# Kernel optimization log

Measured on AMD Instinct MI355X. Metric: run time of the kernel, lower is better.

## Reference

```python
import jax, jax.numpy as jnp
import numpy as np

B, T, C, H = 2, 2048, 1024, 16
D = C // H  # head dim


def setup_inputs() -> dict:
    key = jax.random.key(0)
    ks = jax.random.split(key, 8)
    s = 1.0 / np.sqrt(C)
    return {
        "x_q": jax.random.normal(ks[0], (B, T, C), jnp.float32),
        "x_kv": jax.random.normal(ks[1], (B, T, C), jnp.float32),
        "Wq": jax.random.normal(ks[2], (C, C), jnp.float32) * s,
        "bq": jnp.zeros((C,), jnp.float32),
        "Wkv": jax.random.normal(ks[3], (C, 2 * C), jnp.float32) * s,
        "bkv": jnp.zeros((2 * C,), jnp.float32),
        "Wo": jax.random.normal(ks[4], (C, C), jnp.float32) * s,
        "bo": jnp.zeros((C,), jnp.float32),
    }


def reference(x_q, x_kv, Wq, bq, Wkv, bkv, Wo, bo):
    q = x_q @ Wq + bq                      # [B,Tq,C]
    kv = x_kv @ Wkv + bkv                  # [B,Tkv,2C]
    k, v = kv[..., :C], kv[..., C:]
    # split heads -> [B,H,T,D]
    q = q.reshape(B, T, H, D).transpose(0, 2, 1, 3)
    k = k.reshape(B, T, H, D).transpose(0, 2, 1, 3)
    v = v.reshape(B, T, H, D).transpose(0, 2, 1, 3)
    att = jnp.einsum("bhqd,bhkd->bhqk", q, k) * (1.0 / np.sqrt(D))
    att = jax.nn.softmax(att, axis=-1)
    y = jnp.einsum("bhqk,bhkd->bhqd", att, v)
    y = y.transpose(0, 2, 1, 3).reshape(B, T, C)
    return y @ Wo + bo
```

## Files before the change

### kernel.cpp

```cpp
#include <hip/hip_runtime.h>

#define NB 2
#define NT 2048
#define NC 1024
#define NH 16
#define ND 64
#define NC2 2048
#define QSCALE (0.125f * 1.4426950408889634f)

typedef __attribute__((ext_vector_type(8))) __bf16 bf16x8;
typedef __attribute__((ext_vector_type(8))) unsigned short ushort8;
typedef __attribute__((ext_vector_type(4))) float f32x4;

__device__ __forceinline__ unsigned short bf16_bits(float f) {
  union { float f; unsigned int u; } x; x.f = f;
  unsigned int r = x.u + 0x7fffu + ((x.u >> 16) & 1u);
  return (unsigned short)(r >> 16);
}
__device__ __forceinline__ float bf2f(unsigned short u) {
  union { unsigned int u; float f; } x; x.u = ((unsigned int)u) << 16;
  return x.f;
}
__device__ __forceinline__ void g2l16(const void* g, void* l) {
  __builtin_amdgcn_global_load_lds(
      (const __attribute__((address_space(1))) unsigned int*)g,
      (__attribute__((address_space(3))) unsigned int*)l, 16, 0, 0);
}
__device__ __forceinline__ bf16x8 ld8(const unsigned short* p) {
  return *(const bf16x8*)p;
}
__device__ __forceinline__ unsigned int cvtpk(float lo, float hi) {
  unsigned int r;
  asm("v_cvt_pk_bf16_f32 %0, %1, %2" : "=v"(r) : "v"(lo), "v"(hi));
  return r;
}
__device__ __forceinline__ float vexp2(float x) {
  float r;
  asm("v_exp_f32 %0, %1" : "=v"(r) : "v"(x));
  return r;
}

__device__ __forceinline__ int wave_is_f32(const unsigned short* __restrict__ x) {
  const int lane = threadIdx.x & 63;
  ulonglong2 v = ((const ulonglong2*)x)[lane];
  const unsigned short* u = (const unsigned short*)&v;
  int c = 0;
#pragma unroll
  for (int k = 0; k < 8; ++k) {
    int e = (u[k] >> 7) & 0xFF;
    c += (e != 0 && (e < 112 || e > 142)) ? 1 : 0;
  }
#pragma unroll
  for (int off = 32; off > 0; off >>= 1) c += __shfl_down(c, off);
  return __shfl(c, 0) > 64;
}

__global__ __launch_bounds__(256) void prep(const void* __restrict__ xq,
                                            const void* __restrict__ xkv,
                                            const void* __restrict__ w0,
                                            const void* __restrict__ w1,
                                            const void* __restrict__ w2,
                                            unsigned short* __restrict__ oq,
                                            unsigned short* __restrict__ okv,
                                            unsigned short* __restrict__ o0,
                                            unsigned short* __restrict__ o1,
                                            unsigned short* __restrict__ o2) {
  __shared__ unsigned short tile[32][33];
  const int bx = blockIdx.x, by = blockIdx.y;
  const int f = wave_is_f32((const unsigned short*)xq);
  if (bx < 128) {
    if (!f) return;
    const int fb = bx * 32 + by;
    const void* in = (fb < 2048) ? xq : xkv;
    unsigned short* out = (fb < 2048) ? oq : okv;
    const int i = (fb & 2047) * 256 + threadIdx.x;
    const float4* p = (const float4*)in;
    float4 a = p[i * 2], b = p[i * 2 + 1];
    ushort8 o;
    o[0] = bf16_bits(a.x); o[1] = bf16_bits(a.y); o[2] = bf16_bits(a.z); o[3] = bf16_bits(a.w);
    o[4] = bf16_bits(b.x); o[5] = bf16_bits(b.y); o[6] = bf16_bits(b.z); o[7] = bf16_bits(b.w);
    *(ushort8*)&out[(size_t)i * 8] = o;
  } else {
    const int tb = bx - 128;
    const void* in; unsigned short* out; int cols, cb;
    if (tb < 32)      { in = w0; out = o0; cols = NC;  cb = tb; }
    else if (tb < 96) { in = w1; out = o1; cols = NC2; cb = tb - 32; }
    else              { in = w2; out = o2; cols = NC;  cb = tb - 96; }
    const int c0 = cb * 32, r0 = by * 32;
    const int tx = threadIdx.x & 31, ty = threadIdx.x >> 5;
#pragma unroll
    for (int i = 0; i < 32; i += 8) {
      size_t idx = (size_t)(r0 + ty + i) * cols + c0 + tx;
      tile[ty + i][tx] = f ? bf16_bits(((const float*)in)[idx]) : ((const unsigned short*)in)[idx];
    }
    __syncthreads();
#pragma unroll
    for (int i = 0; i < 32; i += 8)
      out[(size_t)(c0 + ty + i) * NC + r0 + tx] = tile[tx][ty + i];
  }
}

__global__ __launch_bounds__(256) void gemm_qkv(const unsigned short* __restrict__ xq_raw,
                                                const unsigned short* __restrict__ xkv_raw,
                                                const unsigned short* __restrict__ xq_cvt,
                                                const unsigned short* __restrict__ xkv_cvt,
                                                const unsigned short* __restrict__ Wqt,
                                                const unsigned short* __restrict__ Wkvt,
                                                const void* __restrict__ bq,
                                                const void* __restrict__ bkv,
                                                unsigned short* __restrict__ qb,
                                                unsigned short* __restrict__ kf2,
                                                unsigned short* __restrict__ vt2) {
  __shared__ unsigned short As[128][64];
  __shared__ unsigned short Bs[128][64];
  const int f = wave_is_f32(xq_raw);
  const bool isq = blockIdx.y < 8;
  const unsigned short* A  = isq ? (f ? xq_cvt : xq_raw) : (f ? xkv_cvt : xkv_raw);
  const unsigned short* Bt = isq ? Wqt : Wkvt;
  const int m0 = blockIdx.x * 128;
  const int n0 = (isq ? blockIdx.y : blockIdx.y - 8) * 128;
  const int tid = threadIdx.x, w = tid >> 6, lane = tid & 63;
  const int lrow = lane & 15, lhi = lane >> 4;
  const int wr = w >> 1, wc = w & 1;
  const int grow = lane >> 3;
  const int gc = (((lane & 7) ^ grow) * 8);
  const int rg = (lrow & 7);
  f32x4 acc[4][4] = {};
  for (int k0 = 0; k0 < NC; k0 += 64) {
    __syncthreads();
#pragma unroll
    for (int p = 0; p < 4; ++p) {
      const int r = w * 32 + p * 8;
      g2l16(&A[(size_t)(m0 + r + grow) * NC + k0 + gc], &As[r][0]);
      g2l16(&Bt[(size_t)(n0 + r + grow) * NC + k0 + gc], &Bs[r][0]);
    }
    __syncthreads();
    bf16x8 af[2][4], bfr[2][4];
#pragma unroll
    for (int kk = 0; kk < 2; ++kk) {
#pragma unroll
      for (int i = 0; i < 4; ++i)
        af[kk][i] = ld8(&As[wr * 64 + i * 16 + lrow][((kk * 4 + lhi) ^ rg) * 8]);
#pragma unroll
      for (int j = 0; j < 4; ++j)
        bfr[kk][j] = ld8(&Bs[wc * 64 + j * 16 + lrow][((kk * 4 + lhi) ^ rg) * 8]);
    }
#pragma unroll
    for (int kk = 0; kk < 2; ++kk)
#pragma unroll
      for (int i = 0; i < 4; ++i)
#pragma unroll
        for (int j = 0; j < 4; ++j)
          acc[i][j] = __builtin_amdgcn_mfma_f32_16x16x32_bf16(af[kk][i], bfr[kk][j], acc[i][j], 0, 0, 0);
  }
  const void* bias = isq ? bq : bkv;
  if (!isq && n0 >= NC) {
#pragma unroll
    for (int j = 0; j < 4; ++j) {
      const int col = n0 + wc * 64 + j * 16 + lrow;
      const float bj = f ? ((const float*)bias)[col] : bf2f(((const unsigned short*)bias)[col]);
#pragma unroll
      for (int i = 0; i < 4; ++i) {
        const int row = m0 + wr * 64 + i * 16 + lhi * 4;
        float v[4];
#pragma unroll
        for (int r = 0; r < 4; ++r) v[r] = acc[i][j][r] + bj;
        const int cv = col - NC;
        const int hV = cv >> 6, dcol = cv & 63;
        const int bV = row >> 11, tt = row & 2047;
        const size_t base = ((size_t)((bV * NH + hV) * 32 + (tt >> 6))) * 4096
                          + (dcol >> 4) * 1024 + ((tt >> 4) & 1) * 512
                          + (((tt >> 2) & 3) * 16 + (dcol & 15)) * 8 + ((tt >> 5) & 1) * 4;
        ushort4 o4;
        o4.x = bf16_bits(v[0]); o4.y = bf16_bits(v[1]);
        o4.z = bf16_bits(v[2]); o4.w = bf16_bits(v[3]);
        *(ushort4*)&vt2[base] = o4;
      }
    }
  } else {
    __syncthreads();
    unsigned short* Cw = &As[0][0] + w * 1280;
    const int rowbase = m0 + wr * 64;
    const int hK = (n0 + wc * 64) >> 6;
    const size_t tb = ((size_t)(((rowbase >> 11) * NH + hK) * 32 + ((rowbase & 2047) >> 6))) * 4096;
#pragma unroll
    for (int i = 0; i < 4; ++i) {
#pragma unroll
      for (int j = 0; j < 4; ++j) {
        const int col = n0 + wc * 64 + j * 16 + lrow;
        const float bj = f ? ((const float*)bias)[col] : bf2f(((const unsigned short*)bias)[col]);
#pragma unroll
        for (int r = 0; r < 4; ++r) {
          const float v = acc[i][j][r] + bj;
          Cw[(lhi * 4 + r) * 72 + j * 16 + lrow] = bf16_bits(isq ? v * QSCALE : v);
        }
      }
      if (isq) {
#pragma unroll
        for (int p = 0; p < 2; ++p) {
          const int row_l = p * 8 + (lane >> 3), col_l = (lane & 7) * 8;
          const bf16x8 v8 = ld8(&Cw[row_l * 72 + col_l]);
          *(bf16x8*)&qb[(size_t)(rowbase + i * 16 + row_l) * NC + n0 + wc * 64 + col_l] = v8;
        }
      } else {
#pragma unroll
        for (int p = 0; p < 2; ++p) {
          const bf16x8 v8 = ld8(&Cw[(lane & 15) * 72 + p * 32 + (lane >> 4) * 8]);
          *(bf16x8*)&kf2[tb + i * 1024 + p * 512 + lane * 8] = v8;
        }
      }
    }
  }
}

__global__ __launch_bounds__(256) void gemm_out(const unsigned short* __restrict__ A,
                                                const unsigned short* __restrict__ Bt,
                                                const void* __restrict__ bias,
                                                void* __restrict__ Cout,
                                                const unsigned short* __restrict__ xdet) {
  __shared__ unsigned short As[128][64];
  __shared__ unsigned short Bs[128][64];
  const int f = wave_is_f32(xdet);
  const int m0 = blockIdx.x * 128, n0 = blockIdx.y * 128;
  const int tid = threadIdx.x, w = tid >> 6, lane = tid & 63;
  const int lrow = lane & 15, lhi = lane >> 4;
  const int wr = w >> 1, wc = w & 1;
  const int grow = lane >> 3;
  const int gc = (((lane & 7) ^ grow) * 8);
  const int rg = (lrow & 7);
  f32x4 acc[4][4] = {};
  for (int k0 = 0; k0 < NC; k0 += 64) {
    __syncthreads();
#pragma unroll
    for (int p = 0; p < 4; ++p) {
      const int r = w * 32 + p * 8;
      g2l16(&A[(size_t)(m0 + r + grow) * NC + k0 + gc], &As[r][0]);
      g2l16(&Bt[(size_t)(n0 + r + grow) * NC + k0 + gc], &Bs[r][0]);
    }
    __syncthreads();
    bf16x8 af[2][4], bfr[2][4];
#pragma unroll
    for (int kk = 0; kk < 2; ++kk) {
#pragma unroll
      for (int i = 0; i < 4; ++i)
        af[kk][i] = ld8(&As[wr * 64 + i * 16 + lrow][((kk * 4 + lhi) ^ rg) * 8]);
#pragma unroll
      for (int j = 0; j < 4; ++j)
        bfr[kk][j] = ld8(&Bs[wc * 64 + j * 16 + lrow][((kk * 4 + lhi) ^ rg) * 8]);
    }
#pragma unroll
    for (int kk = 0; kk < 2; ++kk)
#pragma unroll
      for (int i = 0; i < 4; ++i)
#pragma unroll
        for (int j = 0; j < 4; ++j)
          acc[i][j] = __builtin_amdgcn_mfma_f32_16x16x32_bf16(af[kk][i], bfr[kk][j], acc[i][j], 0, 0, 0);
  }
#pragma unroll
  for (int j = 0; j < 4; ++j) {
    const int col = n0 + wc * 64 + j * 16 + lrow;
    const float bj = f ? ((const float*)bias)[col] : bf2f(((const unsigned short*)bias)[col]);
#pragma unroll
    for (int i = 0; i < 4; ++i) {
      const int row = m0 + wr * 64 + i * 16 + lhi * 4;
#pragma unroll
      for (int r = 0; r < 4; ++r) {
        const float v = acc[i][j][r] + bj;
        const size_t idx = (size_t)(row + r) * NC + col;
        if (f) ((float*)Cout)[idx] = v;
        else ((unsigned short*)Cout)[idx] = bf16_bits(v);
      }
    }
  }
}

__global__ __launch_bounds__(64) void flash_attn(const unsigned short* __restrict__ q,
                                                 const unsigned short* __restrict__ kf2,
                                                 const unsigned short* __restrict__ vt2,
                                                 unsigned short* __restrict__ y) {
  const int fid = blockIdx.x + (blockIdx.y << 5);
  const int swz = ((fid & 7) << 7) + (fid >> 3);
  const int qt = swz & 31, bh = swz >> 5;
  const int b = bh >> 4, h = bh & 15;
  const int lane = threadIdx.x;
  const int lq = lane & 15, lhi = lane >> 4;

  bf16x8 qf0[2], qf1[2], qf2[2], qf3[2];
  {
    const unsigned short* qp = q + (size_t)(b * NT + qt * 64 + lq) * NC + h * ND + lhi * 8;
    qf0[0] = ld8(qp);                      qf0[1] = ld8(qp + 32);
    qf1[0] = ld8(qp + (size_t)16 * NC);    qf1[1] = ld8(qp + (size_t)16 * NC + 32);
    qf2[0] = ld8(qp + (size_t)32 * NC);    qf2[1] = ld8(qp + (size_t)32 * NC + 32);
    qf3[0] = ld8(qp + (size_t)48 * NC);    qf3[1] = ld8(qp + (size_t)48 * NC + 32);
  }
  f32x4 acc0[4] = {}, acc1[4] = {}, acc2[4] = {}, acc3[4] = {};
  float l0 = 0.f, l1 = 0.f, l2 = 0.f, l3 = 0.f;
  const unsigned short* kbase = kf2 + ((size_t)bh * 32) * 4096 + (size_t)lane * 8;
  const unsigned short* vbase = vt2 + ((size_t)bh * 32) * 4096 + (size_t)lane * 8;

  bf16x8 kR[4][2], vR[4][2];
#define KLOAD(kt_)                                                              \
  {                                                                             \
    _Pragma("unroll") for (int j = 0; j < 4; ++j)                               \
      _Pragma("unroll") for (int kk = 0; kk < 2; ++kk)                          \
        kR[j][kk] = ld8(kbase + (size_t)(kt_)*4096 + j * 1024 + kk * 512);      \
  }
#define VLOAD(kt_)                                                              \
  {                                                                             \
    _Pragma("unroll") for (int jd = 0; jd < 4; ++jd)                            \
      _Pragma("unroll") for (int jj = 0; jj < 2; ++jj)                          \
        vR[jd][jj] = ld8(vbase + (size_t)(kt_)*4096 + jd * 1024 + jj * 512);    \
  }
#define GROUP(QF_, ACC_, L_)                                                      \
  {                                                                               \
    f32x4 s0 = {}, s1 = {}, s2 = {}, s3 = {};                                     \
    s0 = __builtin_amdgcn_mfma_f32_16x16x32_bf16(kR[0][0], QF_[0], s0, 0, 0, 0);  \
    s0 = __builtin_amdgcn_mfma_f32_16x16x32_bf16(kR[0][1], QF_[1], s0, 0, 0, 0);  \
    s1 = __builtin_amdgcn_mfma_f32_16x16x32_bf16(kR[1][0], QF_[0], s1, 0, 0, 0);  \
    s1 = __builtin_amdgcn_mfma_f32_16x16x32_bf16(kR[1][1], QF_[1], s1, 0, 0, 0);  \
    s2 = __builtin_amdgcn_mfma_f32_16x16x32_bf16(kR[2][0], QF_[0], s2, 0, 0, 0);  \
    s2 = __builtin_amdgcn_mfma_f32_16x16x32_bf16(kR[2][1], QF_[1], s2, 0, 0, 0);  \
    s3 = __builtin_amdgcn_mfma_f32_16x16x32_bf16(kR[3][0], QF_[0], s3, 0, 0, 0);  \
    s3 = __builtin_amdgcn_mfma_f32_16x16x32_bf16(kR[3][1], QF_[1], s3, 0, 0, 0);  \
    float rs = 0.f;                                                               \
    _Pragma("unroll") for (int r = 0; r < 4; ++r) {                               \
      s0[r] = vexp2(s0[r]); rs += s0[r];                                          \
      s1[r] = vexp2(s1[r]); rs += s1[r];                                          \
      s2[r] = vexp2(s2[r]); rs += s2[r];                                          \
      s3[r] = vexp2(s3[r]); rs += s3[r];                                          \
    }                                                                             \
    rs += __shfl_xor(rs, 16); rs += __shfl_xor(rs, 32);                           \
    L_ += rs;                                                                     \
    union U { unsigned int u[4]; bf16x8 v; };                                     \
    U p0, p1;                                                                     \
    p0.u[0] = cvtpk(s0[0], s0[1]); p0.u[1] = cvtpk(s0[2], s0[3]);                 \
    p0.u[2] = cvtpk(s2[0], s2[1]); p0.u[3] = cvtpk(s2[2], s2[3]);                 \
    p1.u[0] = cvtpk(s1[0], s1[1]); p1.u[1] = cvtpk(s1[2], s1[3]);                 \
    p1.u[2] = cvtpk(s3[0], s3[1]); p1.u[3] = cvtpk(s3[2], s3[3]);                 \
    __builtin_amdgcn_s_setprio(1);                                                \
    _Pragma("unroll") for (int jd = 0; jd < 4; ++jd) {                            \
      ACC_[jd] = __builtin_amdgcn_mfma_f32_16x16x32_bf16(vR[jd][0], p0.v, ACC_[jd], 0, 0, 0); \
      ACC_[jd] = __builtin_amdgcn_mfma_f32_16x16x32_bf16(vR[jd][1], p1.v, ACC_[jd], 0, 0, 0); \
    }                                                                             \
    __builtin_amdgcn_s_setprio(0);                                                \
  }

  KLOAD(0);
  VLOAD(0);
  for (int kt = 0; kt < 32; ++kt) {
    GROUP(qf0, acc0, l0);
    GROUP(qf1, acc1, l1);
    GROUP(qf2, acc2, l2);
    {
      f32x4 s0 = {}, s1 = {}, s2 = {}, s3 = {};
      s0 = __builtin_amdgcn_mfma_f32_16x16x32_bf16(kR[0][0], qf3[0], s0, 0, 0, 0);
      s0 = __builtin_amdgcn_mfma_f32_16x16x32_bf16(kR[0][1], qf3[1], s0, 0, 0, 0);
      s1 = __builtin_amdgcn_mfma_f32_16x16x32_bf16(kR[1][0], qf3[0], s1, 0, 0, 0);
      s1 = __builtin_amdgcn_mfma_f32_16x16x32_bf16(kR[1][1], qf3[1], s1, 0, 0, 0);
      s2 = __builtin_amdgcn_mfma_f32_16x16x32_bf16(kR[2][0], qf3[0], s2, 0, 0, 0);
      s2 = __builtin_amdgcn_mfma_f32_16x16x32_bf16(kR[2][1], qf3[1], s2, 0, 0, 0);
      s3 = __builtin_amdgcn_mfma_f32_16x16x32_bf16(kR[3][0], qf3[0], s3, 0, 0, 0);
      s3 = __builtin_amdgcn_mfma_f32_16x16x32_bf16(kR[3][1], qf3[1], s3, 0, 0, 0);
      if (kt + 1 < 32) KLOAD(kt + 1);
      float rs = 0.f;
#pragma unroll
      for (int r = 0; r < 4; ++r) {
        s0[r] = vexp2(s0[r]); rs += s0[r];
        s1[r] = vexp2(s1[r]); rs += s1[r];
        s2[r] = vexp2(s2[r]); rs += s2[r];
        s3[r] = vexp2(s3[r]); rs += s3[r];
      }
      rs += __shfl_xor(rs, 16); rs += __shfl_xor(rs, 32);
      l3 += rs;
      union U { unsigned int u[4]; bf16x8 v; };
      U p0, p1;
      p0.u[0] = cvtpk(s0[0], s0[1]); p0.u[1] = cvtpk(s0[2], s0[3]);
      p0.u[2] = cvtpk(s2[0], s2[1]); p0.u[3] = cvtpk(s2[2], s2[3]);
      p1.u[0] = cvtpk(s1[0], s1[1]); p1.u[1] = cvtpk(s1[2], s1[3]);
      p1.u[2] = cvtpk(s3[0], s3[1]); p1.u[3] = cvtpk(s3[2], s3[3]);
      __builtin_amdgcn_s_setprio(1);
#pragma unroll
      for (int jd = 0; jd < 4; ++jd) {
        acc3[jd] = __builtin_amdgcn_mfma_f32_16x16x32_bf16(vR[jd][0], p0.v, acc3[jd], 0, 0, 0);
        acc3[jd] = __builtin_amdgcn_mfma_f32_16x16x32_bf16(vR[jd][1], p1.v, acc3[jd], 0, 0, 0);
      }
      __builtin_amdgcn_s_setprio(0);
    }
    if (kt + 1 < 32) VLOAD(kt + 1);
  }
#undef KLOAD
#undef VLOAD
#undef GROUP

  const float i0 = 1.f / l0, i1 = 1.f / l1, i2 = 1.f / l2, i3 = 1.f / l3;
  const size_t base0 = (size_t)(b * NT + qt * 64 + lq) * NC + h * ND + lhi * 4;
#pragma unroll
  for (int jd = 0; jd < 4; ++jd) {
    uint2 o;
    o.x = cvtpk(acc0[jd][0] * i0, acc0[jd][1] * i0);
    o.y = cvtpk(acc0[jd][2] * i0, acc0[jd][3] * i0);
    *(uint2*)&y[base0 + jd * 16] = o;
    o.x = cvtpk(acc1[jd][0] * i1, acc1[jd][1] * i1);
    o.y = cvtpk(acc1[jd][2] * i1, acc1[jd][3] * i1);
    *(uint2*)&y[base0 + (size_t)16 * NC + jd * 16] = o;
    o.x = cvtpk(acc2[jd][0] * i2, acc2[jd][1] * i2);
    o.y = cvtpk(acc2[jd][2] * i2, acc2[jd][3] * i2);
    *(uint2*)&y[base0 + (size_t)32 * NC + jd * 16] = o;
    o.x = cvtpk(acc3[jd][0] * i3, acc3[jd][1] * i3);
    o.y = cvtpk(acc3[jd][2] * i3, acc3[jd][3] * i3);
    *(uint2*)&y[base0 + (size_t)48 * NC + jd * 16] = o;
  }
}

extern "C" void kernel_launch(void* const* d_in, const int* in_sizes, int n_in,
                              void* d_out, int out_size, void* d_ws, size_t ws_size,
                              hipStream_t stream) {
  (void)in_sizes; (void)n_in; (void)out_size; (void)ws_size;
  char* ws = (char*)d_ws;
  unsigned short* xq_b  = (unsigned short*)(ws);
  unsigned short* xkv_b = (unsigned short*)(ws + ((size_t)8  << 20));
  unsigned short* Wqt   = (unsigned short*)(ws + ((size_t)16 << 20));
  unsigned short* Wkvt  = (unsigned short*)(ws + ((size_t)18 << 20));
  unsigned short* Wot   = (unsigned short*)(ws + ((size_t)22 << 20));
  unsigned short* qb    = (unsigned short*)(ws + ((size_t)24 << 20));
  unsigned short* kf2   = (unsigned short*)(ws + ((size_t)32 << 20));
  unsigned short* vt2   = (unsigned short*)(ws + ((size_t)48 << 20));
  unsigned short* yb    = (unsigned short*)(ws + ((size_t)56 << 20));
  const unsigned short* xdet = (const unsigned short*)d_in[0];

  prep<<<dim3(256, 32), 256, 0, stream>>>(d_in[0], d_in[1], d_in[2], d_in[4], d_in[6],
                                          xq_b, xkv_b, Wqt, Wkvt, Wot);
  gemm_qkv<<<dim3(32, 24), 256, 0, stream>>>((const unsigned short*)d_in[0],
                                             (const unsigned short*)d_in[1],
                                             xq_b, xkv_b, Wqt, Wkvt, d_in[3], d_in[5],
                                             qb, kf2, vt2);
  flash_attn<<<dim3(32, 32), 64, 0, stream>>>(qb, kf2, vt2, yb);
  gemm_out<<<dim3(32, 8), 256, 0, stream>>>(yb, Wot, d_in[7], d_out, xdet);
}
```

Baseline: 136.7 us.

## Rewrite QKV GEMM as 256x256 tile, 512-thread, double-buffered LDS pipeline

```diff
diff --git a/kernel.cpp b/kernel.cpp
--- a/kernel.cpp
+++ b/kernel.cpp
@@ -100,73 +100,118 @@
   }
 }
 
-__global__ __launch_bounds__(256) void gemm_qkv(const unsigned short* __restrict__ xq_raw,
-                                                const unsigned short* __restrict__ xkv_raw,
-                                                const unsigned short* __restrict__ xq_cvt,
-                                                const unsigned short* __restrict__ xkv_cvt,
-                                                const unsigned short* __restrict__ Wqt,
-                                                const unsigned short* __restrict__ Wkvt,
-                                                const void* __restrict__ bq,
-                                                const void* __restrict__ bkv,
-                                                unsigned short* __restrict__ qb,
-                                                unsigned short* __restrict__ kf2,
-                                                unsigned short* __restrict__ vt2) {
-  __shared__ unsigned short As[128][64];
-  __shared__ unsigned short Bs[128][64];
+__global__ __launch_bounds__(512) void gemm_qkv256(const unsigned short* __restrict__ xq_raw,
+                                                   const unsigned short* __restrict__ xkv_raw,
+                                                   const unsigned short* __restrict__ xq_cvt,
+                                                   const unsigned short* __restrict__ xkv_cvt,
+                                                   const unsigned short* __restrict__ Wqt,
+                                                   const unsigned short* __restrict__ Wkvt,
+                                                   const void* __restrict__ bq,
+                                                   const void* __restrict__ bkv,
+                                                   unsigned short* __restrict__ qb,
+                                                   unsigned short* __restrict__ kf2,
+                                                   unsigned short* __restrict__ vt2) {
+  extern __shared__ char smem[];
   const int f = wave_is_f32(xq_raw);
-  const bool isq = blockIdx.y < 8;
+  const int bx = blockIdx.x, by = blockIdx.y;
+  const bool isq = by < 4;
   const unsigned short* A  = isq ? (f ? xq_cvt : xq_raw) : (f ? xkv_cvt : xkv_raw);
   const unsigned short* Bt = isq ? Wqt : Wkvt;
-  const int m0 = blockIdx.x * 128;
-  const int n0 = (isq ? blockIdx.y : blockIdx.y - 8) * 128;
+  const int m0 = bx * 256;
+  const int n0 = (isq ? by : by - 4) * 256;
   const int tid = threadIdx.x, w = tid >> 6, lane = tid & 63;
-  const int lrow = lane & 15, lhi = lane >> 4;
-  const int wr = w >> 1, wc = w & 1;
-  const int grow = lane >> 3;
-  const int gc = (((lane & 7) ^ grow) * 8);
-  const int rg = (lrow & 7);
-  f32x4 acc[4][4] = {};
-  for (int k0 = 0; k0 < NC; k0 += 64) {
-    __syncthreads();
-#pragma unroll
-    for (int p = 0; p < 4; ++p) {
-      const int r = w * 32 + p * 8;
-      g2l16(&A[(size_t)(m0 + r + grow) * NC + k0 + gc], &As[r][0]);
-      g2l16(&Bt[(size_t)(n0 + r + grow) * NC + k0 + gc], &Bs[r][0]);
-    }
-    __syncthreads();
-    bf16x8 af[2][4], bfr[2][4];
-#pragma unroll
-    for (int kk = 0; kk < 2; ++kk) {
-#pragma unroll
-      for (int i = 0; i < 4; ++i)
-        af[kk][i] = ld8(&As[wr * 64 + i * 16 + lrow][((kk * 4 + lhi) ^ rg) * 8]);
-#pragma unroll
-      for (int j = 0; j < 4; ++j)
-        bfr[kk][j] = ld8(&Bs[wc * 64 + j * 16 + lrow][((kk * 4 + lhi) ^ rg) * 8]);
-    }
-#pragma unroll
-    for (int kk = 0; kk < 2; ++kk)
-#pragma unroll
-      for (int i = 0; i < 4; ++i)
-#pragma unroll
-        for (int j = 0; j < 4; ++j)
-          acc[i][j] = __builtin_amdgcn_mfma_f32_16x16x32_bf16(af[kk][i], bfr[kk][j], acc[i][j], 0, 0, 0);
-  }
+  const int lq = lane & 15, lhi = lane >> 4;
+  const int wr = w >> 2, wc = w & 3;
+  f32x4 acc[8][4] = {};
+
+#define STAGE_HALF(kt_, bf_, sel_)                                                   \
+  {                                                                                  \
+    const unsigned short* G_ = ((sel_) < 2) ? A : Bt;                                \
+    const int r0_ = ((sel_) < 2) ? m0 : n0;                                          \
+    const int h_ = (sel_) & 1;                                                       \
+    char* db_ = smem + (bf_)*65536 + ((sel_) >> 1) * 32768 + h_ * 16384;             \
+    _Pragma("unroll") for (int q_ = 0; q_ < 2; ++q_) {                               \
+      const int o_ = w * 1024 + lane * 16 + q_ * 8192;                               \
+      const int os_ = o_ ^ (((o_ >> 9) & 1) << 5);                                   \
+      g2l16((const char*)G_ +                                                        \
+                ((size_t)(r0_ + h_ * 128 + (os_ >> 7)) * NC + (kt_)*64) * 2 +        \
+                (os_ & 127),                                                         \
+            db_ + w * 1024 + q_ * 8192);                                             \
+    }                                                                                \
+  }
+
+  STAGE_HALF(0, 0, 0);
+  STAGE_HALF(0, 0, 1);
+  STAGE_HALF(0, 0, 2);
+  STAGE_HALF(0, 0, 3);
+  asm volatile("s_waitcnt vmcnt(0)");
+  __builtin_amdgcn_sched_barrier(0);
+  __builtin_amdgcn_s_barrier();
+
+  for (int T = 0; T < 16; ++T) {
+    const int c = T & 1;
+    const char* Ah = smem + c * 65536 + wr * 16384;
+    const char* Bh = smem + c * 65536 + 32768 + (wc >> 1) * 16384;
+    const int brh = (wc & 1) * 64;
+    bf16x8 bF[2][4];
+#pragma unroll
+    for (int ph = 0; ph < 4; ++ph) {
+      if (ph == 0) {
+#pragma unroll
+        for (int kk = 0; kk < 2; ++kk)
+#pragma unroll
+          for (int fj = 0; fj < 4; ++fj) {
+            const int rowh = brh + fj * 16 + lq;
+            const int o = rowh * 128 + kk * 64 + lhi * 16;
+            bF[kk][fj] = ld8((const unsigned short*)(Bh + (o ^ (((o >> 9) & 1) << 5))));
+          }
+      }
+      bf16x8 aF[2][2];
+#pragma unroll
+      for (int kk = 0; kk < 2; ++kk)
+#pragma unroll
+        for (int ii = 0; ii < 2; ++ii) {
+          const int rowh = (ph * 2 + ii) * 16 + lq;
+          const int o = rowh * 128 + kk * 64 + lhi * 16;
+          aF[kk][ii] = ld8((const unsigned short*)(Ah + (o ^ (((o >> 9) & 1) << 5))));
+        }
+      if (T < 15) STAGE_HALF(T + 1, c ^ 1, ph);
+      __builtin_amdgcn_s_barrier();
+      __builtin_amdgcn_s_setprio(1);
+#pragma unroll
+      for (int kk = 0; kk < 2; ++kk)
+#pragma unroll
+        for (int ii = 0; ii < 2; ++ii)
+#pragma unroll
+          for (int fj = 0; fj < 4; ++fj)
+            acc[ph * 2 + ii][fj] =
+                __builtin_amdgcn_mfma_f32_16x16x32_bf16(aF[kk][ii], bF[kk][fj],
+                                                        acc[ph * 2 + ii][fj], 0, 0, 0);
+      __builtin_amdgcn_s_setprio(0);
+    }
+    asm volatile("s_waitcnt vmcnt(0)");
+    __builtin_amdgcn_sched_barrier(0);
+    __builtin_amdgcn_s_barrier();
+  }
+#undef STAGE_HALF
+
   const void* bias = isq ? bq : bkv;
-  if (!isq && n0 >= NC) {
-#pragma unroll
-    for (int j = 0; j < 4; ++j) {
-      const int col = n0 + wc * 64 + j * 16 + lrow;
-      const float bj = f ? ((const float*)bias)[col] : bf2f(((const unsigned short*)bias)[col]);
-#pragma unroll
-      for (int i = 0; i < 4; ++i) {
-        const int row = m0 + wr * 64 + i * 16 + lhi * 4;
+  const int rowbase = m0 + wr * 128;
+  unsigned short* Cw = (unsigned short*)(smem + w * 2304);
+  if (by >= 8) {
+    const int n0v = (by - 8) * 256;
+#pragma unroll
+    for (int fj = 0; fj < 4; ++fj) {
+      const int cv = n0v + wc * 64 + fj * 16 + lq;
+      const float bj = f ? ((const float*)bias)[NC + cv]
+                         : bf2f(((const unsigned short*)bias)[NC + cv]);
+      const int hV = cv >> 6, dcol = cv & 63;
+#pragma unroll
+      for (int fi = 0; fi < 8; ++fi) {
+        const int row = rowbase + fi * 16 + lhi * 4;
         float v[4];
 #pragma unroll
-        for (int r = 0; r < 4; ++r) v[r] = acc[i][j][r] + bj;
-        const int cv = col - NC;
-        const int hV = cv >> 6, dcol = cv & 63;
+        for (int r = 0; r < 4; ++r) v[r] = acc[fi][fj][r] + bj;
         const int bV = row >> 11, tt = row & 2047;
         const size_t base = ((size_t)((bV * NH + hV) * 32 + (tt >> 6))) * 4096
                           + (dcol >> 4) * 1024 + ((tt >> 4) & 1) * 512
@@ -178,21 +223,17 @@
       }
     }
   } else {
-    __syncthreads();
-    unsigned short* Cw = &As[0][0] + w * 1280;
-    const int rowbase = m0 + wr * 64;
-    const int hK = (n0 + wc * 64) >> 6;
-    const size_t tb = ((size_t)(((rowbase >> 11) * NH + hK) * 32 + ((rowbase & 2047) >> 6))) * 4096;
-#pragma unroll
-    for (int i = 0; i < 4; ++i) {
-#pragma unroll
-      for (int j = 0; j < 4; ++j) {
-        const int col = n0 + wc * 64 + j * 16 + lrow;
+    const int hK = ((by - 4) << 2) + wc;
+#pragma unroll
+    for (int fi = 0; fi < 8; ++fi) {
+#pragma unroll
+      for (int fj = 0; fj < 4; ++fj) {
+        const int col = n0 + wc * 64 + fj * 16 + lq;
         const float bj = f ? ((const float*)bias)[col] : bf2f(((const unsigned short*)bias)[col]);
 #pragma unroll
         for (int r = 0; r < 4; ++r) {
-          const float v = acc[i][j][r] + bj;
-          Cw[(lhi * 4 + r) * 72 + j * 16 + lrow] = bf16_bits(isq ? v * QSCALE : v);
+          const float v = acc[fi][fj][r] + bj;
+          Cw[(lhi * 4 + r) * 72 + fj * 16 + lq] = bf16_bits(isq ? v * QSCALE : v);
         }
       }
       if (isq) {
@@ -200,13 +241,17 @@
         for (int p = 0; p < 2; ++p) {
           const int row_l = p * 8 + (lane >> 3), col_l = (lane & 7) * 8;
           const bf16x8 v8 = ld8(&Cw[row_l * 72 + col_l]);
-          *(bf16x8*)&qb[(size_t)(rowbase + i * 16 + row_l) * NC + n0 + wc * 64 + col_l] = v8;
+          *(bf16x8*)&qb[(size_t)(rowbase + fi * 16 + row_l) * NC + n0 + wc * 64 + col_l] = v8;
         }
       } else {
+        const int rowglob = rowbase + fi * 16;
+        const int bK = rowglob >> 11, tt = rowglob & 2047;
+        const size_t tb = ((size_t)((bK * NH + hK) * 32 + (tt >> 6))) * 4096
+                        + ((tt >> 4) & 3) * 1024;
 #pragma unroll
         for (int p = 0; p < 2; ++p) {
           const bf16x8 v8 = ld8(&Cw[(lane & 15) * 72 + p * 32 + (lane >> 4) * 8]);
-          *(bf16x8*)&kf2[tb + i * 1024 + p * 512 + lane * 8] = v8;
+          *(bf16x8*)&kf2[tb + p * 512 + lane * 8] = v8;
         }
       }
     }
@@ -428,12 +473,19 @@
   unsigned short* yb    = (unsigned short*)(ws + ((size_t)56 << 20));
   const unsigned short* xdet = (const unsigned short*)d_in[0];
 
+  static bool attr_set = false;
+  if (!attr_set) {
+    hipFuncSetAttribute((const void*)gemm_qkv256,
+                        hipFuncAttributeMaxDynamicSharedMemorySize, 131072);
+    attr_set = true;
+  }
+
   prep<<<dim3(256, 32), 256, 0, stream>>>(d_in[0], d_in[1], d_in[2], d_in[4], d_in[6],
                                           xq_b, xkv_b, Wqt, Wkvt, Wot);
-  gemm_qkv<<<dim3(32, 24), 256, 0, stream>>>((const unsigned short*)d_in[0],
-                                             (const unsigned short*)d_in[1],
-                                             xq_b, xkv_b, Wqt, Wkvt, d_in[3], d_in[5],
-                                             qb, kf2, vt2);
+  gemm_qkv256<<<dim3(16, 12), 512, 131072, stream>>>((const unsigned short*)d_in[0],
+                                                     (const unsigned short*)d_in[1],
+                                                     xq_b, xkv_b, Wqt, Wkvt,
+                                                     d_in[3], d_in[5], qb, kf2, vt2);
   flash_attn<<<dim3(32, 32), 64, 0, stream>>>(qb, kf2, vt2, yb);
   gemm_out<<<dim3(32, 8), 256, 0, stream>>>(yb, Wot, d_in[7], d_out, xdet);
 }
```

Result: faster. 127.3 us (-6.9%).
